# Kernel tuning notes

Measured on AMD Instinct MI355X. Metric: run time of the kernel, lower is better.

Reference implementation:

```python
import jax, jax.numpy as jnp
import numpy as np

D_MODEL = 1024
NUM_HEADS = 16
HEAD_DIM = D_MODEL // NUM_HEADS
B, S = 2, 2048


def setup_inputs() -> dict:
    key = jax.random.key(0)
    ks = jax.random.split(key, 7)
    scale = 1.0 / np.sqrt(D_MODEL)
    return {
        "query": jax.random.normal(ks[0], (B, S, D_MODEL), jnp.float32),
        "key": jax.random.normal(ks[1], (B, S, D_MODEL), jnp.float32),
        "value": jax.random.normal(ks[2], (B, S, D_MODEL), jnp.float32),
        "Wq": jax.random.normal(ks[3], (D_MODEL, D_MODEL), jnp.float32) * scale,
        "Wk": jax.random.normal(ks[4], (D_MODEL, D_MODEL), jnp.float32) * scale,
        "Wv": jax.random.normal(ks[5], (D_MODEL, D_MODEL), jnp.float32) * scale,
        "Wo": jax.random.normal(ks[6], (D_MODEL, D_MODEL), jnp.float32) * scale,
    }


def reference(query, key, value, Wq, Wk, Wv, Wo):
    b, tl, _ = query.shape
    sl = key.shape[1]
    # Linear (no bias): x @ W.T, then split heads -> (B, H, L, Dh)
    def split_heads(x, L):
        return x.reshape(b, L, NUM_HEADS, HEAD_DIM).transpose(0, 2, 1, 3)
    Q = split_heads(query @ Wq.T, tl)
    K = split_heads(key @ Wk.T, sl)
    V = split_heads(value @ Wv.T, sl)
    scores = jnp.einsum("bhqd,bhkd->bhqk", Q, K) / jnp.sqrt(jnp.float32(HEAD_DIM))
    attn_weights = jax.nn.softmax(scores, axis=-1)
    # dropout is identity in eval mode
    context = jnp.einsum("bhqk,bhkd->bhqd", attn_weights, V)
    context = context.transpose(0, 2, 1, 3).reshape(b, tl, D_MODEL)
    output = context @ Wo.T
    return (output, attn_weights)
```

## Files before the change

### kernel.cpp

```cpp
#include <hip/hip_runtime.h>
#include <stdint.h>
#include <stddef.h>

#define D_MODEL 1024
#define NHEADS  16
#define HDIM    64
#define BB      2
#define SSEQ    2048

using bf16x8 = __attribute__((ext_vector_type(8))) short;
using f32x4  = __attribute__((ext_vector_type(4))) float;
using s16x4  = __attribute__((ext_vector_type(4))) short;

static __device__ __forceinline__ float b2f(short s) {
  union { float f; unsigned u; } v;
  v.u = ((unsigned)(unsigned short)s) << 16;
  return v.f;
}
static __device__ __forceinline__ short f2b(float f) {
  union { float f; unsigned u; } v;
  v.f = f;
  unsigned r = v.u + 0x7fffu + ((v.u >> 16) & 1u);
  return (short)(r >> 16);
}

static __device__ __forceinline__ void gload16(const void* g, void* l) {
  __builtin_amdgcn_global_load_lds(
      (const __attribute__((address_space(1))) unsigned int*)g,
      (__attribute__((address_space(3))) unsigned int*)l, 16, 0, 0);
}

__global__ __launch_bounds__(256) void k_cvt(const float* __restrict__ src,
                                             short* __restrict__ dst, int n4) {
  int i = blockIdx.x * blockDim.x + threadIdx.x;
  const int stride = gridDim.x * blockDim.x;
  for (; i < n4; i += stride) {
    const float4 v = ((const float4*)src)[i];
    s16x4 o;
    o[0] = f2b(v.x); o[1] = f2b(v.y); o[2] = f2b(v.z); o[3] = f2b(v.w);
    ((s16x4*)dst)[i] = o;
  }
}

template <bool F32OUT>
static __device__ __forceinline__ void gemm_bt_dev(
    const short* __restrict__ A, const short* __restrict__ W, void* __restrict__ Cv,
    int N, int K) {
  __shared__ short sA[128 * 32];
  __shared__ short sB[128 * 32];

  const int t  = threadIdx.x;
  const int l  = t & 63;
  const int w  = t >> 6;
  const int wm = w >> 1, wn = w & 1;
  const int g  = l >> 4, lr = l & 15;
  const int m0 = blockIdx.y * 128;
  const int n0 = blockIdx.x * 128;

  f32x4 acc[4][4];
#pragma unroll
  for (int i = 0; i < 4; ++i)
#pragma unroll
    for (int j = 0; j < 4; ++j) {
      acc[i][j][0] = 0.f; acc[i][j][1] = 0.f;
      acc[i][j][2] = 0.f; acc[i][j][3] = 0.f;
    }

  const int r0 = t >> 2;
  const int c0 = (t & 3) * 8;
  const short* ga0 = A + (size_t)(m0 + r0) * K + c0;
  const short* ga1 = A + (size_t)(m0 + 64 + r0) * K + c0;
  const short* gb0 = W + (size_t)(n0 + r0) * K + c0;
  const short* gb1 = W + (size_t)(n0 + 64 + r0) * K + c0;
  short* la0 = &sA[(t & ~63) * 8];
  short* la1 = la0 + 256 * 8;
  short* lb0 = &sB[(t & ~63) * 8];
  short* lb1 = lb0 + 256 * 8;

  for (int k0 = 0; k0 < K; k0 += 32) {
    __syncthreads();
    gload16(ga0 + k0, la0);
    gload16(ga1 + k0, la1);
    gload16(gb0 + k0, lb0);
    gload16(gb1 + k0, lb1);
    __syncthreads();

    bf16x8 af[4], bfr[4];
#pragma unroll
    for (int i = 0; i < 4; ++i)
      af[i] = *(const bf16x8*)&sA[(wm * 64 + i * 16 + lr) * 32 + g * 8];
#pragma unroll
    for (int i = 0; i < 4; ++i)
      bfr[i] = *(const bf16x8*)&sB[(wn * 64 + i * 16 + lr) * 32 + g * 8];
#pragma unroll
    for (int i = 0; i < 4; ++i)
#pragma unroll
      for (int j = 0; j < 4; ++j)
        acc[i][j] = __builtin_amdgcn_mfma_f32_16x16x32_bf16(af[i], bfr[j],
                                                            acc[i][j], 0, 0, 0);
  }

#pragma unroll
  for (int i = 0; i < 4; ++i)
#pragma unroll
    for (int j = 0; j < 4; ++j)
#pragma unroll
      for (int rr = 0; rr < 4; ++rr) {
        const int row = m0 + wm * 64 + i * 16 + g * 4 + rr;
        const int col = n0 + wn * 64 + j * 16 + lr;
        if (F32OUT)
          ((float*)Cv)[(size_t)row * N + col] = acc[i][j][rr];
        else
          ((short*)Cv)[(size_t)row * N + col] = f2b(acc[i][j][rr]);
      }
}

__global__ __launch_bounds__(256) void k_gemm_f32out(
    const short* __restrict__ A, const short* __restrict__ W,
    float* __restrict__ C, int N, int K) {
  gemm_bt_dev<true>(A, W, C, N, K);
}

__global__ __launch_bounds__(256) void k_gemm_qkv(
    const short* __restrict__ q, const short* __restrict__ k,
    const short* __restrict__ v, const short* __restrict__ wq,
    const short* __restrict__ wk, const short* __restrict__ wv,
    short* __restrict__ Qb, short* __restrict__ Kb, short* __restrict__ Vb) {
  const short *A, *W;
  short* C;
  if (blockIdx.z == 0)      { A = q; W = wq; C = Qb; }
  else if (blockIdx.z == 1) { A = k; W = wk; C = Kb; }
  else                      { A = v; W = wv; C = Vb; }
  gemm_bt_dev<false>(A, W, C, D_MODEL, D_MODEL);
}

__global__ __launch_bounds__(256) void k_transpose_v(
    const short* __restrict__ Vb, short* __restrict__ Vt) {
  __shared__ short tile[64][66];
  const int bh = blockIdx.x;
  const int b = bh >> 4, h = bh & 15;
  const int s0 = blockIdx.y * 64;
  const int t = threadIdx.x;
#pragma unroll
  for (int i = 0; i < 16; ++i) {
    int e = t + i * 256;
    int si = e >> 6, dj = e & 63;
    tile[si][dj] = Vb[((size_t)b * SSEQ + s0 + si) * D_MODEL + h * HDIM + dj];
  }
  __syncthreads();
#pragma unroll
  for (int i = 0; i < 16; ++i) {
    int e = t + i * 256;
    int dj = e >> 6, si = e & 63;
    Vt[((size_t)bh * HDIM + dj) * SSEQ + s0 + si] = tile[si][dj];
  }
}

__global__ __launch_bounds__(256) void k_attn(
    const short* __restrict__ Qb, const short* __restrict__ Kb,
    const short* __restrict__ Vt, float* __restrict__ attnO,
    short* __restrict__ ctx) {
  __shared__ __attribute__((aligned(16))) short ptile[4][16][40];
  __shared__ float wmx[4][16];
  __shared__ float wls[4][16];
  __shared__ f32x4 red[4][4][64];

  const int t = threadIdx.x;
  const int l = t & 63, w = t >> 6;
  const int g = l >> 4, lr = l & 15;
  const int orig = blockIdx.x;
  const int id = (orig & 7) * 512 + (orig >> 3);
  const int q0 = (id & 127) * 16;
  const int bh = id >> 7;
  const int b = bh >> 4, h = bh & 15;

  const size_t qoff = ((size_t)b * SSEQ + q0 + lr) * D_MODEL + h * HDIM;
  const bf16x8 aq0 = *(const bf16x8*)&Qb[qoff + g * 8];
  const bf16x8 aq1 = *(const bf16x8*)&Qb[qoff + 32 + g * 8];

  const short* Kh = Kb + (size_t)b * SSEQ * D_MODEL + h * HDIM;
  const short* Vh = Vt + (size_t)bh * HDIM * SSEQ;
  const int kbase = w * 512;

  float pm[4], pl[4];
#pragma unroll
  for (int rr = 0; rr < 4; ++rr) { pm[rr] = -1e30f; pl[rr] = 0.f; }

  for (int st = 0; st < 16; ++st) {
    const int n0 = kbase + st * 32;
    const short* kr0 = Kh + (size_t)(n0 + lr) * D_MODEL;
    const short* kr1 = Kh + (size_t)(n0 + 16 + lr) * D_MODEL;
    const bf16x8 ka0 = *(const bf16x8*)&kr0[g * 8];
    const bf16x8 ka1 = *(const bf16x8*)&kr0[32 + g * 8];
    const bf16x8 kb0 = *(const bf16x8*)&kr1[g * 8];
    const bf16x8 kb1 = *(const bf16x8*)&kr1[32 + g * 8];
    f32x4 sA, sB;
    sA[0] = 0.f; sA[1] = 0.f; sA[2] = 0.f; sA[3] = 0.f;
    sB[0] = 0.f; sB[1] = 0.f; sB[2] = 0.f; sB[3] = 0.f;
    sA = __builtin_amdgcn_mfma_f32_16x16x32_bf16(aq0, ka0, sA, 0, 0, 0);
    sA = __builtin_amdgcn_mfma_f32_16x16x32_bf16(aq1, ka1, sA, 0, 0, 0);
    sB = __builtin_amdgcn_mfma_f32_16x16x32_bf16(aq0, kb0, sB, 0, 0, 0);
    sB = __builtin_amdgcn_mfma_f32_16x16x32_bf16(aq1, kb1, sB, 0, 0, 0);
#pragma unroll
    for (int rr = 0; rr < 4; ++rr) {
      const float s1 = sA[rr] * 0.125f;
      const float s2 = sB[rr] * 0.125f;
      const float nm = fmaxf(pm[rr], fmaxf(s1, s2));
      pl[rr] = pl[rr] * __expf(pm[rr] - nm) + __expf(s1 - nm) + __expf(s2 - nm);
      pm[rr] = nm;
    }
  }
#pragma unroll
  for (int mask = 1; mask < 16; mask <<= 1) {
#pragma unroll
    for (int rr = 0; rr < 4; ++rr) {
      const float om = __shfl_xor(pm[rr], mask, 64);
      const float ol = __shfl_xor(pl[rr], mask, 64);
      const float nm = fmaxf(pm[rr], om);
      pl[rr] = pl[rr] * __expf(pm[rr] - nm) + ol * __expf(om - nm);
      pm[rr] = nm;
    }
  }
  if (lr == 0) {
#pragma unroll
    for (int rr = 0; rr < 4; ++rr) {
      wmx[w][g * 4 + rr] = pm[rr];
      wls[w][g * 4 + rr] = pl[rr];
    }
  }
  __syncthreads();

  float M[4], inv[4];
#pragma unroll
  for (int rr = 0; rr < 4; ++rr) {
    const int row = g * 4 + rr;
    const float m0 = wmx[0][row], m1 = wmx[1][row];
    const float m2 = wmx[2][row], m3 = wmx[3][row];
    const float Mv = fmaxf(fmaxf(m0, m1), fmaxf(m2, m3));
    const float L = wls[0][row] * __expf(m0 - Mv) + wls[1][row] * __expf(m1 - Mv) +
                    wls[2][row] * __expf(m2 - Mv) + wls[3][row] * __expf(m3 - Mv);
    M[rr] = Mv;
    inv[rr] = 1.f / L;
  }

  f32x4 accO[4];
#pragma unroll
  for (int u = 0; u < 4; ++u) {
    accO[u][0] = 0.f; accO[u][1] = 0.f; accO[u][2] = 0.f; accO[u][3] = 0.f;
  }
  float* arow0 = attnO + ((size_t)bh * SSEQ + q0) * SSEQ;

  for (int st = 0; st < 16; ++st) {
    const int n0 = kbase + st * 32;
    const short* kr0 = Kh + (size_t)(n0 + lr) * D_MODEL;
    const short* kr1 = Kh + (size_t)(n0 + 16 + lr) * D_MODEL;
    const bf16x8 ka0 = *(const bf16x8*)&kr0[g * 8];
    const bf16x8 ka1 = *(const bf16x8*)&kr0[32 + g * 8];
    const bf16x8 kb0 = *(const bf16x8*)&kr1[g * 8];
    const bf16x8 kb1 = *(const bf16x8*)&kr1[32 + g * 8];
    bf16x8 bv[4];
#pragma unroll
    for (int u = 0; u < 4; ++u)
      bv[u] = *(const bf16x8*)&Vh[(size_t)(u * 16 + lr) * SSEQ + n0 + g * 8];

    f32x4 sA, sB;
    sA[0] = 0.f; sA[1] = 0.f; sA[2] = 0.f; sA[3] = 0.f;
    sB[0] = 0.f; sB[1] = 0.f; sB[2] = 0.f; sB[3] = 0.f;
    sA = __builtin_amdgcn_mfma_f32_16x16x32_bf16(aq0, ka0, sA, 0, 0, 0);
    sA = __builtin_amdgcn_mfma_f32_16x16x32_bf16(aq1, ka1, sA, 0, 0, 0);
    sB = __builtin_amdgcn_mfma_f32_16x16x32_bf16(aq0, kb0, sB, 0, 0, 0);
    sB = __builtin_amdgcn_mfma_f32_16x16x32_bf16(aq1, kb1, sB, 0, 0, 0);

#pragma unroll
    for (int rr = 0; rr < 4; ++rr) {
      const int row = g * 4 + rr;
      const float pa = __expf(sA[rr] * 0.125f - M[rr]) * inv[rr];
      const float pb = __expf(sB[rr] * 0.125f - M[rr]) * inv[rr];
      arow0[(size_t)row * SSEQ + n0 + lr] = pa;
      arow0[(size_t)row * SSEQ + n0 + 16 + lr] = pb;
      ptile[w][row][lr] = f2b(pa);
      ptile[w][row][16 + lr] = f2b(pb);
    }
    const bf16x8 ap = *(const bf16x8*)&ptile[w][lr][g * 8];
#pragma unroll
    for (int u = 0; u < 4; ++u)
      accO[u] = __builtin_amdgcn_mfma_f32_16x16x32_bf16(ap, bv[u], accO[u], 0, 0, 0);
  }

#pragma unroll
  for (int u = 0; u < 4; ++u) red[w][u][l] = accO[u];
  __syncthreads();
  {
    f32x4 o = red[0][w][l];
    const f32x4 o1 = red[1][w][l], o2 = red[2][w][l], o3 = red[3][w][l];
    o[0] += o1[0] + o2[0] + o3[0];
    o[1] += o1[1] + o2[1] + o3[1];
    o[2] += o1[2] + o2[2] + o3[2];
    o[3] += o1[3] + o2[3] + o3[3];
#pragma unroll
    for (int rr = 0; rr < 4; ++rr) {
      const int qr = q0 + g * 4 + rr;
      ctx[((size_t)b * SSEQ + qr) * D_MODEL + h * HDIM + w * 16 + lr] =
          f2b(o[rr]);
    }
  }
}

extern "C" void kernel_launch(void* const* d_in, const int* in_sizes, int n_in,
                              void* d_out, int out_size, void* d_ws,
                              size_t ws_size, hipStream_t stream) {
  const float* qf  = (const float*)d_in[0];
  const float* kf  = (const float*)d_in[1];
  const float* vf  = (const float*)d_in[2];
  const float* wqf = (const float*)d_in[3];
  const float* wkf = (const float*)d_in[4];
  const float* wvf = (const float*)d_in[5];
  const float* wof = (const float*)d_in[6];

  float* out  = (float*)d_out;
  float* attn = out + (size_t)BB * SSEQ * D_MODEL;

  const size_t NTOK = (size_t)BB * SSEQ;
  const size_t XN = NTOK * D_MODEL;
  const size_t WN = (size_t)D_MODEL * D_MODEL;

  short* qb  = (short*)d_ws;
  short* kb  = qb + XN;
  short* vb  = kb + XN;
  short* wqb = vb + XN;
  short* wkb = wqb + WN;
  short* wvb = wkb + WN;
  short* wob = wvb + WN;
  short* Qb  = wob + WN;
  short* Kb  = Qb + XN;
  short* Vb  = Kb + XN;
  short* Vt  = Vb + XN;
  short* ctx = Vt + XN;

  k_cvt<<<512, 256, 0, stream>>>(qf, qb, (int)(XN / 4));
  k_cvt<<<512, 256, 0, stream>>>(kf, kb, (int)(XN / 4));
  k_cvt<<<512, 256, 0, stream>>>(vf, vb, (int)(XN / 4));
  k_cvt<<<256, 256, 0, stream>>>(wqf, wqb, (int)(WN / 4));
  k_cvt<<<256, 256, 0, stream>>>(wkf, wkb, (int)(WN / 4));
  k_cvt<<<256, 256, 0, stream>>>(wvf, wvb, (int)(WN / 4));
  k_cvt<<<256, 256, 0, stream>>>(wof, wob, (int)(WN / 4));

  k_gemm_qkv<<<dim3(D_MODEL / 128, NTOK / 128, 3), 256, 0, stream>>>(
      qb, kb, vb, wqb, wkb, wvb, Qb, Kb, Vb);
  k_transpose_v<<<dim3(BB * NHEADS, SSEQ / 64), 256, 0, stream>>>(Vb, Vt);
  k_attn<<<4096, 256, 0, stream>>>(Qb, Kb, Vt, attn, ctx);
  k_gemm_f32out<<<dim3(D_MODEL / 128, NTOK / 128), 256, 0, stream>>>(
      ctx, wob, out, D_MODEL, D_MODEL);
}
```

Measured before the change: 956.0 us.

## Cache bf16-rounded scores in registers and transpose QK tile for vector stores

The first pass now keeps the scaled QK scores, rounded to bf16 and packed two per register, in a 64-entry register array. The second pass reuses them instead of reloading K and recomputing the QK MFMAs. The MFMA operands are swapped so each lane owns one query row, which reduces per-row softmax state to a scalar and lets attention probabilities be written as float4 stores. This trades more VGPR pressure, and so possibly lower occupancy, for removing redundant K loads and matmuls. Rounding scores to bf16 also changes the attention weights slightly.

```diff
diff --git a/kernel.cpp b/kernel.cpp
--- a/kernel.cpp
+++ b/kernel.cpp
@@ -22,6 +22,22 @@
   v.f = f;
   unsigned r = v.u + 0x7fffu + ((v.u >> 16) & 1u);
   return (short)(r >> 16);
+}
+static __device__ __forceinline__ unsigned rnd2(float a, float b, float* fa,
+                                                float* fb) {
+  union { float f; unsigned u; } x, y;
+  x.f = a; y.f = b;
+  const unsigned ra = (x.u + 0x7fffu + ((x.u >> 16) & 1u)) & 0xffff0000u;
+  const unsigned rb = (y.u + 0x7fffu + ((y.u >> 16) & 1u)) & 0xffff0000u;
+  x.u = ra; y.u = rb;
+  *fa = x.f; *fb = y.f;
+  return (ra >> 16) | rb;
+}
+static __device__ __forceinline__ float unlo(unsigned u) {
+  union { float f; unsigned v; } x; x.v = u << 16; return x.f;
+}
+static __device__ __forceinline__ float unhi(unsigned u) {
+  union { float f; unsigned v; } x; x.v = u & 0xffff0000u; return x.f;
 }
 
 static __device__ __forceinline__ void gload16(const void* g, void* l) {
@@ -182,10 +198,9 @@
   const short* Vh = Vt + (size_t)bh * HDIM * SSEQ;
   const int kbase = w * 512;
 
-  float pm[4], pl[4];
-#pragma unroll
-  for (int rr = 0; rr < 4; ++rr) { pm[rr] = -1e30f; pl[rr] = 0.f; }
-
+  unsigned sreg[64];
+  float pm = -1e30f, pl = 0.f;
+#pragma unroll
   for (int st = 0; st < 16; ++st) {
     const int n0 = kbase + st * 32;
     const short* kr0 = Kh + (size_t)(n0 + lr) * D_MODEL;
@@ -197,50 +212,43 @@
     f32x4 sA, sB;
     sA[0] = 0.f; sA[1] = 0.f; sA[2] = 0.f; sA[3] = 0.f;
     sB[0] = 0.f; sB[1] = 0.f; sB[2] = 0.f; sB[3] = 0.f;
-    sA = __builtin_amdgcn_mfma_f32_16x16x32_bf16(aq0, ka0, sA, 0, 0, 0);
-    sA = __builtin_amdgcn_mfma_f32_16x16x32_bf16(aq1, ka1, sA, 0, 0, 0);
-    sB = __builtin_amdgcn_mfma_f32_16x16x32_bf16(aq0, kb0, sB, 0, 0, 0);
-    sB = __builtin_amdgcn_mfma_f32_16x16x32_bf16(aq1, kb1, sB, 0, 0, 0);
-#pragma unroll
-    for (int rr = 0; rr < 4; ++rr) {
-      const float s1 = sA[rr] * 0.125f;
-      const float s2 = sB[rr] * 0.125f;
-      const float nm = fmaxf(pm[rr], fmaxf(s1, s2));
-      pl[rr] = pl[rr] * __expf(pm[rr] - nm) + __expf(s1 - nm) + __expf(s2 - nm);
-      pm[rr] = nm;
-    }
-  }
-#pragma unroll
-  for (int mask = 1; mask < 16; mask <<= 1) {
-#pragma unroll
-    for (int rr = 0; rr < 4; ++rr) {
-      const float om = __shfl_xor(pm[rr], mask, 64);
-      const float ol = __shfl_xor(pl[rr], mask, 64);
-      const float nm = fmaxf(pm[rr], om);
-      pl[rr] = pl[rr] * __expf(pm[rr] - nm) + ol * __expf(om - nm);
-      pm[rr] = nm;
-    }
-  }
-  if (lr == 0) {
-#pragma unroll
-    for (int rr = 0; rr < 4; ++rr) {
-      wmx[w][g * 4 + rr] = pm[rr];
-      wls[w][g * 4 + rr] = pl[rr];
-    }
-  }
+    sA = __builtin_amdgcn_mfma_f32_16x16x32_bf16(ka0, aq0, sA, 0, 0, 0);
+    sA = __builtin_amdgcn_mfma_f32_16x16x32_bf16(ka1, aq1, sA, 0, 0, 0);
+    sB = __builtin_amdgcn_mfma_f32_16x16x32_bf16(kb0, aq0, sB, 0, 0, 0);
+    sB = __builtin_amdgcn_mfma_f32_16x16x32_bf16(kb1, aq1, sB, 0, 0, 0);
+    float v0, v1, v2, v3, v4, v5, v6, v7;
+    sreg[st * 4 + 0] = rnd2(sA[0] * 0.125f, sA[1] * 0.125f, &v0, &v1);
+    sreg[st * 4 + 1] = rnd2(sA[2] * 0.125f, sA[3] * 0.125f, &v2, &v3);
+    sreg[st * 4 + 2] = rnd2(sB[0] * 0.125f, sB[1] * 0.125f, &v4, &v5);
+    sreg[st * 4 + 3] = rnd2(sB[2] * 0.125f, sB[3] * 0.125f, &v6, &v7);
+    const float mx = fmaxf(fmaxf(fmaxf(v0, v1), fmaxf(v2, v3)),
+                           fmaxf(fmaxf(v4, v5), fmaxf(v6, v7)));
+    const float nm = fmaxf(pm, mx);
+    const float s = __expf(v0 - nm) + __expf(v1 - nm) + __expf(v2 - nm) +
+                    __expf(v3 - nm) + __expf(v4 - nm) + __expf(v5 - nm) +
+                    __expf(v6 - nm) + __expf(v7 - nm);
+    pl = pl * __expf(pm - nm) + s;
+    pm = nm;
+  }
+#pragma unroll
+  for (int mask = 16; mask <= 32; mask <<= 1) {
+    const float om = __shfl_xor(pm, mask, 64);
+    const float ol = __shfl_xor(pl, mask, 64);
+    const float nm = fmaxf(pm, om);
+    pl = pl * __expf(pm - nm) + ol * __expf(om - nm);
+    pm = nm;
+  }
+  if (l < 16) { wmx[w][lr] = pm; wls[w][lr] = pl; }
   __syncthreads();
 
-  float M[4], inv[4];
-#pragma unroll
-  for (int rr = 0; rr < 4; ++rr) {
-    const int row = g * 4 + rr;
-    const float m0 = wmx[0][row], m1 = wmx[1][row];
-    const float m2 = wmx[2][row], m3 = wmx[3][row];
-    const float Mv = fmaxf(fmaxf(m0, m1), fmaxf(m2, m3));
-    const float L = wls[0][row] * __expf(m0 - Mv) + wls[1][row] * __expf(m1 - Mv) +
-                    wls[2][row] * __expf(m2 - Mv) + wls[3][row] * __expf(m3 - Mv);
-    M[rr] = Mv;
-    inv[rr] = 1.f / L;
+  float M, inv;
+  {
+    const float m0 = wmx[0][lr], m1 = wmx[1][lr];
+    const float m2 = wmx[2][lr], m3 = wmx[3][lr];
+    M = fmaxf(fmaxf(m0, m1), fmaxf(m2, m3));
+    const float L = wls[0][lr] * __expf(m0 - M) + wls[1][lr] * __expf(m1 - M) +
+                    wls[2][lr] * __expf(m2 - M) + wls[3][lr] * __expf(m3 - M);
+    inv = 1.f / L;
   }
 
   f32x4 accO[4];
@@ -248,43 +256,43 @@
   for (int u = 0; u < 4; ++u) {
     accO[u][0] = 0.f; accO[u][1] = 0.f; accO[u][2] = 0.f; accO[u][3] = 0.f;
   }
-  float* arow0 = attnO + ((size_t)bh * SSEQ + q0) * SSEQ;
-
+  float* arow = attnO + ((size_t)bh * SSEQ + q0 + lr) * SSEQ;
+
+#pragma unroll
   for (int st = 0; st < 16; ++st) {
     const int n0 = kbase + st * 32;
-    const short* kr0 = Kh + (size_t)(n0 + lr) * D_MODEL;
-    const short* kr1 = Kh + (size_t)(n0 + 16 + lr) * D_MODEL;
-    const bf16x8 ka0 = *(const bf16x8*)&kr0[g * 8];
-    const bf16x8 ka1 = *(const bf16x8*)&kr0[32 + g * 8];
-    const bf16x8 kb0 = *(const bf16x8*)&kr1[g * 8];
-    const bf16x8 kb1 = *(const bf16x8*)&kr1[32 + g * 8];
-    bf16x8 bv[4];
-#pragma unroll
-    for (int u = 0; u < 4; ++u)
-      bv[u] = *(const bf16x8*)&Vh[(size_t)(u * 16 + lr) * SSEQ + n0 + g * 8];
-
-    f32x4 sA, sB;
-    sA[0] = 0.f; sA[1] = 0.f; sA[2] = 0.f; sA[3] = 0.f;
-    sB[0] = 0.f; sB[1] = 0.f; sB[2] = 0.f; sB[3] = 0.f;
-    sA = __builtin_amdgcn_mfma_f32_16x16x32_bf16(aq0, ka0, sA, 0, 0, 0);
-    sA = __builtin_amdgcn_mfma_f32_16x16x32_bf16(aq1, ka1, sA, 0, 0, 0);
-    sB = __builtin_amdgcn_mfma_f32_16x16x32_bf16(aq0, kb0, sB, 0, 0, 0);
-    sB = __builtin_amdgcn_mfma_f32_16x16x32_bf16(aq1, kb1, sB, 0, 0, 0);
-
-#pragma unroll
-    for (int rr = 0; rr < 4; ++rr) {
-      const int row = g * 4 + rr;
-      const float pa = __expf(sA[rr] * 0.125f - M[rr]) * inv[rr];
-      const float pb = __expf(sB[rr] * 0.125f - M[rr]) * inv[rr];
-      arow0[(size_t)row * SSEQ + n0 + lr] = pa;
-      arow0[(size_t)row * SSEQ + n0 + 16 + lr] = pb;
-      ptile[w][row][lr] = f2b(pa);
-      ptile[w][row][16 + lr] = f2b(pb);
-    }
+    const bf16x8 bv0 = *(const bf16x8*)&Vh[(size_t)(lr) * SSEQ + n0 + g * 8];
+    const bf16x8 bv1 = *(const bf16x8*)&Vh[(size_t)(16 + lr) * SSEQ + n0 + g * 8];
+    const bf16x8 bv2 = *(const bf16x8*)&Vh[(size_t)(32 + lr) * SSEQ + n0 + g * 8];
+    const bf16x8 bv3 = *(const bf16x8*)&Vh[(size_t)(48 + lr) * SSEQ + n0 + g * 8];
+
+    const unsigned u0 = sreg[st * 4 + 0], u1 = sreg[st * 4 + 1];
+    const unsigned u2 = sreg[st * 4 + 2], u3 = sreg[st * 4 + 3];
+    const float pa0 = __expf(unlo(u0) - M) * inv;
+    const float pa1 = __expf(unhi(u0) - M) * inv;
+    const float pa2 = __expf(unlo(u1) - M) * inv;
+    const float pa3 = __expf(unhi(u1) - M) * inv;
+    const float pa4 = __expf(unlo(u2) - M) * inv;
+    const float pa5 = __expf(unhi(u2) - M) * inv;
+    const float pa6 = __expf(unlo(u3) - M) * inv;
+    const float pa7 = __expf(unhi(u3) - M) * inv;
+
+    float4 s0, s1;
+    s0.x = pa0; s0.y = pa1; s0.z = pa2; s0.w = pa3;
+    s1.x = pa4; s1.y = pa5; s1.z = pa6; s1.w = pa7;
+    *(float4*)(arow + n0 + g * 4) = s0;
+    *(float4*)(arow + n0 + 16 + g * 4) = s1;
+
+    s16x4 h0, h1;
+    h0[0] = f2b(pa0); h0[1] = f2b(pa1); h0[2] = f2b(pa2); h0[3] = f2b(pa3);
+    h1[0] = f2b(pa4); h1[1] = f2b(pa5); h1[2] = f2b(pa6); h1[3] = f2b(pa7);
+    *(s16x4*)&ptile[w][lr][g * 4] = h0;
+    *(s16x4*)&ptile[w][lr][16 + g * 4] = h1;
     const bf16x8 ap = *(const bf16x8*)&ptile[w][lr][g * 8];
-#pragma unroll
-    for (int u = 0; u < 4; ++u)
-      accO[u] = __builtin_amdgcn_mfma_f32_16x16x32_bf16(ap, bv[u], accO[u], 0, 0, 0);
+    accO[0] = __builtin_amdgcn_mfma_f32_16x16x32_bf16(ap, bv0, accO[0], 0, 0, 0);
+    accO[1] = __builtin_amdgcn_mfma_f32_16x16x32_bf16(ap, bv1, accO[1], 0, 0, 0);
+    accO[2] = __builtin_amdgcn_mfma_f32_16x16x32_bf16(ap, bv2, accO[2], 0, 0, 0);
+    accO[3] = __builtin_amdgcn_mfma_f32_16x16x32_bf16(ap, bv3, accO[3], 0, 0, 0);
   }
 
 #pragma unroll
```

After: 886.8 us. 1.08x faster.
